# Performance work log

Measured on AMD Instinct MI355X. Metric: run time of the kernel, lower is better.

## Reference

```python
import jax, jax.numpy as jnp
import numpy as np

EMBED_DIM = 1024


def setup_inputs() -> dict:
    key = jax.random.key(0)
    ks = jax.random.split(key, 9)
    d = EMBED_DIM
    s = 1.0 / np.sqrt(d)
    return {
        "x": jax.random.normal(ks[0], (4, 2048, d), dtype=jnp.float32),
        "wq": jax.random.normal(ks[1], (d, d), dtype=jnp.float32) * s,
        "bq": jnp.zeros((d,), dtype=jnp.float32),
        "wk": jax.random.normal(ks[2], (d, d), dtype=jnp.float32) * s,
        "bk": jnp.zeros((d,), dtype=jnp.float32),
        "wv": jax.random.normal(ks[3], (d, d), dtype=jnp.float32) * s,
        "bv": jnp.zeros((d,), dtype=jnp.float32),
        "wo": jax.random.normal(ks[4], (d, d), dtype=jnp.float32) * s,
        "bo": jnp.zeros((d,), dtype=jnp.float32),
    }


def reference(x, wq, bq, wk, bk, wv, bv, wo, bo):
    # x: [B, S, D]; weights stored as [D_in, D_out] (torch Linear applies x @ W.T,
    # here we fold the transpose into storage).
    d = x.shape[-1]
    q = x @ wq + bq
    k = x @ wk + bk
    v = x @ wv + bv
    scores = jnp.einsum('bqd,bkd->bqk', q, k) / jnp.sqrt(jnp.float32(d))
    attn = jax.nn.softmax(scores, axis=-1)
    out = jnp.einsum('bqk,bkd->bqd', attn, v)
    return out @ wo + bo
```

## Files before the change

### kernel.cpp

```cpp
#include <hip/hip_runtime.h>
#include <stdint.h>

typedef __attribute__((ext_vector_type(4))) float f32x4;
typedef __attribute__((ext_vector_type(8))) short short8v;
typedef __attribute__((ext_vector_type(4))) unsigned short ushort4v;
typedef __attribute__((ext_vector_type(8))) unsigned short ushort8v;

__device__ __forceinline__ unsigned short f2b(float x) {
  union { float f; unsigned int u; } c; c.f = x;
  unsigned int r = (c.u + 0x7fffu + ((c.u >> 16) & 1u)) >> 16;
  return (unsigned short)r;
}

__device__ __forceinline__ void gload_lds16(const void* g, void* l) {
  __builtin_amdgcn_global_load_lds(
      (const __attribute__((address_space(1))) void*)g,
      (__attribute__((address_space(3))) void*)l, 16, 0, 0);
}

__device__ __forceinline__ f32x4 MFMA16(short8v a, short8v b, f32x4 c) {
  return __builtin_amdgcn_mfma_f32_16x16x32_bf16(a, b, c, 0, 0, 0);
}

template <int N>
__device__ __forceinline__ void wvm() {
  if constexpr (N == 8) asm volatile("s_waitcnt vmcnt(8)" ::: "memory");
  else if constexpr (N == 6) asm volatile("s_waitcnt vmcnt(6)" ::: "memory");
  else if constexpr (N == 4) asm volatile("s_waitcnt vmcnt(4)" ::: "memory");
  else if constexpr (N == 3) asm volatile("s_waitcnt vmcnt(3)" ::: "memory");
  else asm volatile("s_waitcnt vmcnt(0)" ::: "memory");
}

__global__ __launch_bounds__(256) void cvt_bf16(const float* __restrict__ in,
                                                unsigned short* __restrict__ out,
                                                int n8) {
  for (int i = blockIdx.x * 256 + threadIdx.x; i < n8; i += gridDim.x * 256) {
    f32x4 a = *((const f32x4*)in + (size_t)i * 2);
    f32x4 b = *((const f32x4*)in + (size_t)i * 2 + 1);
    ushort8v o;
    o[0] = f2b(a[0]); o[1] = f2b(a[1]); o[2] = f2b(a[2]); o[3] = f2b(a[3]);
    o[4] = f2b(b[0]); o[5] = f2b(b[1]); o[6] = f2b(b[2]); o[7] = f2b(b[3]);
    *((ushort8v*)out + i) = o;
  }
}

__global__ __launch_bounds__(256) void wt4_bf16(const float* __restrict__ w0,
                                                const float* __restrict__ w1,
                                                const float* __restrict__ w2,
                                                const float* __restrict__ w3,
                                                unsigned short* __restrict__ o0,
                                                unsigned short* __restrict__ o1,
                                                unsigned short* __restrict__ o2,
                                                unsigned short* __restrict__ o3) {
  const int z = blockIdx.z;
  const float* W = z == 0 ? w0 : z == 1 ? w1 : z == 2 ? w2 : w3;
  unsigned short* WT = z == 0 ? o0 : z == 1 ? o1 : z == 2 ? o2 : o3;
  __shared__ float t[64][65];
  const int bi = blockIdx.y * 64, bj = blockIdx.x * 64;
#pragma unroll
  for (int i = 0; i < 16; ++i) {
    int idx = i * 256 + threadIdx.x;
    int r = idx >> 6, c = idx & 63;
    t[r][c] = W[(size_t)(bi + r) * 1024 + bj + c];
  }
  __syncthreads();
#pragma unroll
  for (int i = 0; i < 16; ++i) {
    int idx = i * 256 + threadIdx.x;
    int r = idx >> 6, c = idx & 63;
    WT[(size_t)(bj + r) * 1024 + bi + c] = f2b(t[c][r]);
  }
}

__global__ __launch_bounds__(256) void softmax_rows(float* __restrict__ S,
                                                    long long bstride) {
  float* row = S + (long long)blockIdx.y * bstride + (size_t)blockIdx.x * 2048;
  const int t = threadIdx.x;
  f32x4 a = *(const f32x4*)(row + t * 8);
  f32x4 b = *(const f32x4*)(row + t * 8 + 4);
  float m = fmaxf(fmaxf(fmaxf(a[0], a[1]), fmaxf(a[2], a[3])),
                  fmaxf(fmaxf(b[0], b[1]), fmaxf(b[2], b[3])));
#pragma unroll
  for (int o = 32; o; o >>= 1) m = fmaxf(m, __shfl_xor(m, o));
  __shared__ float red[4];
  const int wid = t >> 6, lane = t & 63;
  if (lane == 0) red[wid] = m;
  __syncthreads();
  m = fmaxf(fmaxf(red[0], red[1]), fmaxf(red[2], red[3]));
  float e[8];
  float s = 0.f;
#pragma unroll
  for (int j = 0; j < 4; ++j) { e[j] = __expf(a[j] - m); s += e[j]; }
#pragma unroll
  for (int j = 0; j < 4; ++j) { e[4 + j] = __expf(b[j] - m); s += e[4 + j]; }
#pragma unroll
  for (int o = 32; o; o >>= 1) s += __shfl_xor(s, o);
  __syncthreads();
  if (lane == 0) red[wid] = s;
  __syncthreads();
  s = red[0] + red[1] + red[2] + red[3];
  const float inv = 1.f / s;
  ushort8v o8;
#pragma unroll
  for (int j = 0; j < 8; ++j) o8[j] = f2b(e[j] * inv);
  __syncthreads();
  *((ushort8v*)row + t) = o8;
}

__global__ __launch_bounds__(256, 2) void gemm_qkv128(
    const unsigned short* __restrict__ A,
    const unsigned short* __restrict__ B,
    unsigned short* __restrict__ Q, unsigned short* __restrict__ Kp,
    unsigned short* __restrict__ Vt,
    const float* __restrict__ bq, const float* __restrict__ bk,
    const float* __restrict__ bv) {
  __shared__ unsigned short As[128 * 32];
  __shared__ unsigned short Bs[128 * 32];
  const int tid = threadIdx.x;
  const int brow = blockIdx.y * 128, bcol = blockIdx.x * 128;
  const int wid = tid >> 6, lane = tid & 63;
  const int wr = (wid >> 1) * 64, wc = (wid & 1) * 64;
  const int lrow = lane & 15, kblk = lane >> 4;
  f32x4 acc[4][4] = {};
  for (int kk = 0; kk < 1024; kk += 32) {
#pragma unroll
    for (int r = 0; r < 2; ++r) {
      int idx = r * 256 + tid;
      int row = idx >> 2, seg = (idx & 3) * 8;
      gload_lds16(A + (size_t)(brow + row) * 1024 + kk + seg, (char*)As + idx * 16);
      gload_lds16(B + (size_t)(bcol + row) * 1024 + kk + seg, (char*)Bs + idx * 16);
    }
    __syncthreads();
    short8v af[4], bf[4];
#pragma unroll
    for (int m = 0; m < 4; ++m)
      af[m] = *(const short8v*)(As + (wr + m * 16 + lrow) * 32 + kblk * 8);
#pragma unroll
    for (int n = 0; n < 4; ++n)
      bf[n] = *(const short8v*)(Bs + (wc + n * 16 + lrow) * 32 + kblk * 8);
#pragma unroll
    for (int m = 0; m < 4; ++m)
#pragma unroll
      for (int n = 0; n < 4; ++n)
        acc[m][n] = MFMA16(af[m], bf[n], acc[m][n]);
    __syncthreads();
  }
  const int r0 = brow + wr + kblk * 4;
  const int c0 = bcol + wc + lrow;
  const int seg = bcol >> 10;
  if (seg < 2) {
    unsigned short* O = seg == 0 ? Q : Kp;
    const float* bb = seg == 0 ? bq : bk;
#pragma unroll
    for (int m = 0; m < 4; ++m)
#pragma unroll
      for (int n = 0; n < 4; ++n) {
        const int lc = c0 + n * 16 - seg * 1024;
        const float badd = bb[lc];
#pragma unroll
        for (int j = 0; j < 4; ++j)
          O[(size_t)(r0 + m * 16 + j) * 1024 + lc] = f2b(acc[m][n][j] + badd);
      }
  } else {
#pragma unroll
    for (int m = 0; m < 4; ++m)
#pragma unroll
      for (int n = 0; n < 4; ++n) {
        const int lc = c0 + n * 16 - 2048;
        const float badd = bv[lc];
        ushort4v pk;
#pragma unroll
        for (int j = 0; j < 4; ++j) pk[j] = f2b(acc[m][n][j] + badd);
        *(ushort4v*)(Vt + (size_t)lc * 8192 + r0 + m * 16) = pk;
      }
  }
}

template <int EPI, int BM>
__global__ __launch_bounds__(512, 2) void gemm256(
    const unsigned short* __restrict__ A, int lda,
    const unsigned short* __restrict__ B, int ldb,
    void* __restrict__ C0, void* __restrict__ C1, void* __restrict__ C2,
    int ldc, const float* __restrict__ bias0, const float* __restrict__ bias1,
    const float* __restrict__ bias2, float scale, int K,
    long long bsA, long long bsB, long long bsC) {
  extern __shared__ __align__(16) char smem[];
  constexpr int ABY = BM * 64;
  constexpr int KHS = ABY + 16384;
  constexpr int SBUF = 2 * KHS;
  constexpr int MF = BM / 32;
  constexpr int FH = MF / 2;
  constexpr int AL = BM / 128;
  constexpr int L = AL + 2;

  const int tid = threadIdx.x;
  const int z = blockIdx.z;
  A += (long long)z * bsA;
  B += (long long)z * bsB;
  const int blkrow = blockIdx.y * BM, blkcol = blockIdx.x * 256;
  const int lane = tid & 63, wid = tid >> 6;
  const int kblk = lane >> 4, l15 = lane & 15;
  const int arw = (wid >> 2) * (BM / 2) + l15;
  const int brw = (wid & 3) * 64 + l15;
  const int aoff = arw * 64 + ((kblk ^ ((arw >> 1) & 3)) << 4);
  const int boff = ABY + brw * 64 + ((kblk ^ ((brw >> 1) & 3)) << 4);
  const int srow = tid >> 2;
  const int scc = (((tid & 3) ^ ((srow >> 1) & 3)) << 3);
  const unsigned short* ag = A + (size_t)(blkrow + srow) * lda + scc;
  const unsigned short* bg = B + (size_t)(blkcol + srow) * ldb + scc;

  auto stA = [&](char* buf, int kt, int kh) {
    const unsigned short* g = ag + kt * 64 + kh * 32;
    char* l = buf + kh * KHS + tid * 16;
#pragma unroll
    for (int rr = 0; rr < AL; ++rr)
      gload_lds16(g + (size_t)(rr * 128) * lda, l + rr * 8192);
  };
  auto stB = [&](char* buf, int kt, int kh) {
    const unsigned short* g = bg + kt * 64 + kh * 32;
    char* l = buf + ABY + kh * KHS + tid * 16;
    gload_lds16(g, l);
    gload_lds16(g + (size_t)128 * ldb, l + 8192);
  };

  f32x4 acc[MF][4] = {};
  short8v af[4], bf[4];

#define LDAH(BUF, KK, MB)                                                     \
  { _Pragma("unroll") for (int m_ = 0; m_ < FH; ++m_)                         \
      af[m_] = *(const short8v*)((BUF) + (KK)*KHS + aoff + ((MB) + m_) * 1024); }
#define LDB4(BUF, KK)                                                         \
  { _Pragma("unroll") for (int n_ = 0; n_ < 4; ++n_)                          \
      bf[n_] = *(const short8v*)((BUF) + (KK)*KHS + boff + n_ * 1024); }
#define MMH(MH)                                                               \
  { _Pragma("unroll") for (int m_ = 0; m_ < FH; ++m_)                         \
      _Pragma("unroll") for (int n_ = 0; n_ < 4; ++n_)                        \
        acc[(MH)*FH + m_][n_] = MFMA16(af[m_], bf[n_], acc[(MH)*FH + m_][n_]); }
#define BAR __builtin_amdgcn_s_barrier()
#define WLGKM0 asm volatile("s_waitcnt lgkmcnt(0)" ::: "memory")

  const int NT = K >> 6;
  stA(smem, 0, 0); stB(smem, 0, 0); stA(smem, 0, 1); stB(smem, 0, 1);
  wvm<L>();
  BAR;
  for (int t = 0; t < NT; ++t) {
    char* cur = smem + (t & 1) * SBUF;
    char* nxt = smem + ((t + 1) & 1) * SBUF;
    const bool pf = (t + 1 < NT);
    LDAH(cur, 0, 0);
    LDB4(cur, 0);
    if (pf) { stA(nxt, t + 1, 0); stB(nxt, t + 1, 0); }
    BAR; WLGKM0;
    __builtin_amdgcn_s_setprio(1);
    MMH(0);
    __builtin_amdgcn_s_setprio(0);
    BAR;
    LDAH(cur, 0, FH);
    if (pf) { stA(nxt, t + 1, 1); stB(nxt, t + 1, 1); }
    BAR; WLGKM0;
    __builtin_amdgcn_s_setprio(1);
    MMH(1);
    __builtin_amdgcn_s_setprio(0);
    if (pf) wvm<2 * L>(); else wvm<0>();
    BAR;
    LDAH(cur, 1, 0);
    LDB4(cur, 1);
    BAR; WLGKM0;
    __builtin_amdgcn_s_setprio(1);
    MMH(0);
    __builtin_amdgcn_s_setprio(0);
    BAR;
    LDAH(cur, 1, FH);
    BAR; WLGKM0;
    __builtin_amdgcn_s_setprio(1);
    MMH(1);
    __builtin_amdgcn_s_setprio(0);
    if (pf) wvm<L>();
    BAR;
  }

  const int gr0 = blkrow + (wid >> 2) * (BM / 2) + kblk * 4;
  const int gc0 = blkcol + (wid & 3) * 64 + l15;
  if (EPI == 0) {
    float* C = (float*)C0 + (long long)z * bsC;
#pragma unroll
    for (int mi = 0; mi < MF; ++mi)
#pragma unroll
      for (int n = 0; n < 4; ++n) {
        const int gc = gc0 + n * 16;
        const float badd = bias0 ? bias0[gc] : 0.f;
#pragma unroll
        for (int j = 0; j < 4; ++j)
          C[(size_t)(gr0 + mi * 16 + j) * ldc + gc] = acc[mi][n][j] * scale + badd;
      }
  } else if (EPI == 1) {
    unsigned short* C = (unsigned short*)C0 + (long long)z * bsC;
#pragma unroll
    for (int mi = 0; mi < MF; ++mi)
#pragma unroll
      for (int n = 0; n < 4; ++n) {
        const int gc = gc0 + n * 16;
        const float badd = bias0 ? bias0[gc] : 0.f;
#pragma unroll
        for (int j = 0; j < 4; ++j)
          C[(size_t)(gr0 + mi * 16 + j) * ldc + gc] = f2b(acc[mi][n][j] * scale + badd);
      }
  } else {
    const int seg = blkcol >> 10;
#pragma unroll
    for (int mi = 0; mi < MF; ++mi)
#pragma unroll
      for (int n = 0; n < 4; ++n) {
        const int gc = gc0 + n * 16;
        const int lc = gc - seg * 1024;
        if (seg < 2) {
          unsigned short* O = (unsigned short*)(seg == 0 ? C0 : C1);
          const float* bb = (seg == 0 ? bias0 : bias1);
          const float badd = bb[lc];
#pragma unroll
          for (int j = 0; j < 4; ++j)
            O[(size_t)(gr0 + mi * 16 + j) * 1024 + lc] = f2b(acc[mi][n][j] + badd);
        } else {
          unsigned short* O = (unsigned short*)C2;
          const float badd = bias2[lc];
          ushort4v pk;
#pragma unroll
          for (int j = 0; j < 4; ++j) pk[j] = f2b(acc[mi][n][j] + badd);
          *(ushort4v*)(O + (size_t)lc * 8192 + gr0 + mi * 16) = pk;
        }
      }
  }
#undef LDAH
#undef LDB4
#undef MMH
#undef BAR
#undef WLGKM0
}

template <int OMODE, bool BIAS, bool SCALE>
__global__ __launch_bounds__(256, 2) void gemm_bt(
    const unsigned short* __restrict__ A, int lda,
    const unsigned short* __restrict__ B, int ldb,
    void* __restrict__ Cp, int ldc,
    const float* __restrict__ bias, float scale, int K,
    long long bsA, long long bsB, long long bsC) {
  __shared__ unsigned short As[128 * 32];
  __shared__ unsigned short Bs[128 * 32];
  const int tid = threadIdx.x;
  A += (long long)blockIdx.z * bsA;
  B += (long long)blockIdx.z * bsB;
  const int brow = blockIdx.y * 128, bcol = blockIdx.x * 128;
  const int wid = tid >> 6, lane = tid & 63;
  const int wr = (wid >> 1) * 64, wc = (wid & 1) * 64;
  const int lrow = lane & 15, kblk = lane >> 4;
  f32x4 acc[4][4] = {};
  for (int kk = 0; kk < K; kk += 32) {
#pragma unroll
    for (int r = 0; r < 2; ++r) {
      int idx = r * 256 + tid;
      int row = idx >> 2, seg = (idx & 3) * 8;
      gload_lds16(A + (size_t)(brow + row) * lda + kk + seg, (char*)As + idx * 16);
      gload_lds16(B + (size_t)(bcol + row) * ldb + kk + seg, (char*)Bs + idx * 16);
    }
    __syncthreads();
    short8v af[4], bv[4];
#pragma unroll
    for (int m = 0; m < 4; ++m)
      af[m] = *(const short8v*)(As + (wr + m * 16 + lrow) * 32 + kblk * 8);
#pragma unroll
    for (int n = 0; n < 4; ++n)
      bv[n] = *(const short8v*)(Bs + (wc + n * 16 + lrow) * 32 + kblk * 8);
#pragma unroll
    for (int m = 0; m < 4; ++m)
#pragma unroll
      for (int n = 0; n < 4; ++n)
        acc[m][n] = MFMA16(af[m], bv[n], acc[m][n]);
    __syncthreads();
  }
  const int r0 = brow + wr + kblk * 4;
  const int c0 = bcol + wc + lrow;
  if (OMODE == 0) {
    float* C = (float*)Cp + (long long)blockIdx.z * bsC;
#pragma unroll
    for (int m = 0; m < 4; ++m)
#pragma unroll
      for (int n = 0; n < 4; ++n) {
        const int cc = c0 + n * 16;
        const float badd = BIAS ? bias[cc] : 0.f;
#pragma unroll
        for (int j = 0; j < 4; ++j) {
          float v = acc[m][n][j];
          if (SCALE) v *= scale;
          C[(size_t)(r0 + m * 16 + j) * ldc + cc] = v + badd;
        }
      }
  } else if (OMODE == 1) {
    unsigned short* C = (unsigned short*)Cp + (long long)blockIdx.z * bsC;
#pragma unroll
    for (int m = 0; m < 4; ++m)
#pragma unroll
      for (int n = 0; n < 4; ++n) {
        const int cc = c0 + n * 16;
        const float badd = BIAS ? bias[cc] : 0.f;
#pragma unroll
        for (int j = 0; j < 4; ++j) {
          float v = acc[m][n][j];
          if (SCALE) v *= scale;
          C[(size_t)(r0 + m * 16 + j) * ldc + cc] = f2b(v + badd);
        }
      }
  } else {
    unsigned short* C = (unsigned short*)Cp + (long long)blockIdx.z * bsC;
#pragma unroll
    for (int m = 0; m < 4; ++m)
#pragma unroll
      for (int n = 0; n < 4; ++n) {
        const int cc = c0 + n * 16;
        const float badd = BIAS ? bias[cc] : 0.f;
        ushort4v pk;
#pragma unroll
        for (int j = 0; j < 4; ++j) {
          float v = acc[m][n][j];
          if (SCALE) v *= scale;
          pk[j] = f2b(v + badd);
        }
        *(ushort4v*)(C + (size_t)cc * ldc + (r0 + m * 16)) = pk;
      }
  }
}

extern "C" void kernel_launch(void* const* d_in, const int* in_sizes, int n_in,
                              void* d_out, int out_size, void* d_ws, size_t ws_size,
                              hipStream_t stream) {
  const float* x  = (const float*)d_in[0];
  const float* wq = (const float*)d_in[1];
  const float* bq = (const float*)d_in[2];
  const float* wk = (const float*)d_in[3];
  const float* bk = (const float*)d_in[4];
  const float* wv = (const float*)d_in[5];
  const float* bv = (const float*)d_in[6];
  const float* wo = (const float*)d_in[7];
  const float* bo = (const float*)d_in[8];
  float* out = (float*)d_out;
  char* ws = (char*)d_ws;

  const long long WELEM = 1024LL * 1024;
  const long long BATCH = 2048LL * 1024;
  const long long FULL  = 4 * BATCH;
  const long long SELEM = 2048LL * 2048;

  const size_t need_A = 8388608ull + 5ull * 16777216 + 4ull * 16777216;
  const size_t need_C = 8388608ull + 4ull * 4194304 + 16777216ull;

  if (ws_size >= need_A) {
    unsigned short* wqT = (unsigned short*)ws;
    unsigned short* wkT = wqT + WELEM;
    unsigned short* wvT = wkT + WELEM;
    unsigned short* woT = wvT + WELEM;
    unsigned short* xb  = woT + WELEM;
    unsigned short* qb  = xb + FULL;
    unsigned short* kb  = qb + FULL;
    unsigned short* vt  = kb + FULL;
    unsigned short* ao  = vt + FULL;
    float* S = (float*)(ao + FULL);

    hipFuncSetAttribute(reinterpret_cast<const void*>(&gemm256<0, 256>),
                        hipFuncAttributeMaxDynamicSharedMemorySize, 131072);
    hipFuncSetAttribute(reinterpret_cast<const void*>(&gemm256<1, 128>),
                        hipFuncAttributeMaxDynamicSharedMemorySize, 98304);
    hipFuncSetAttribute(reinterpret_cast<const void*>(&gemm256<0, 128>),
                        hipFuncAttributeMaxDynamicSharedMemorySize, 98304);

    cvt_bf16<<<2048, 256, 0, stream>>>(x, xb, (int)(FULL / 8));
    wt4_bf16<<<dim3(16, 16, 4), 256, 0, stream>>>(wq, wk, wv, wo, wqT, wkT, wvT, woT);

    gemm_qkv128<<<dim3(24, 64), 256, 0, stream>>>(
        xb, wqT, qb, kb, vt, bq, bk, bv);
    gemm256<0, 256><<<dim3(8, 8, 4), 512, 131072, stream>>>(
        qb, 1024, kb, 1024, S, nullptr, nullptr, 2048, nullptr, nullptr,
        nullptr, 0.03125f, 1024, BATCH, BATCH, SELEM);
    softmax_rows<<<dim3(2048, 4), 256, 0, stream>>>(S, SELEM);
    gemm256<1, 128><<<dim3(4, 16, 4), 512, 98304, stream>>>(
        (const unsigned short*)S, 4096, vt, 8192, ao, nullptr, nullptr, 1024,
        nullptr, nullptr, nullptr, 1.f, 2048, 2 * SELEM, 2048, BATCH);
    gemm256<0, 128><<<dim3(4, 64, 1), 512, 98304, stream>>>(
        ao, 1024, woT, 1024, out, nullptr, nullptr, 1024, bo, nullptr, nullptr,
        1.f, 1024, 0, 0, 0);
  } else if (ws_size >= need_C) {
    unsigned short* wqT = (unsigned short*)ws;
    unsigned short* wkT = wqT + WELEM;
    unsigned short* wvT = wkT + WELEM;
    unsigned short* woT = wvT + WELEM;
    unsigned short* xb  = woT + WELEM;
    unsigned short* qb  = xb + BATCH;
    unsigned short* kb  = qb + BATCH;
    unsigned short* vtb = kb + BATCH;
    float* S = (float*)(vtb + BATCH);

    wt4_bf16<<<dim3(16, 16, 4), 256, 0, stream>>>(wq, wk, wv, wo, wqT, wkT, wvT, woT);

    for (int b = 0; b < 4; ++b) {
      cvt_bf16<<<1024, 256, 0, stream>>>(x + b * BATCH, xb, (int)(BATCH / 8));
      dim3 gqkv(8, 16);
      gemm_bt<1, true, false><<<gqkv, 256, 0, stream>>>(xb, 1024, wqT, 1024, qb, 1024, bq, 1.f, 1024, 0, 0, 0);
      gemm_bt<1, true, false><<<gqkv, 256, 0, stream>>>(xb, 1024, wkT, 1024, kb, 1024, bk, 1.f, 1024, 0, 0, 0);
      gemm_bt<2, true, false><<<gqkv, 256, 0, stream>>>(xb, 1024, wvT, 1024, vtb, 2048, bv, 1.f, 1024, 0, 0, 0);
      gemm_bt<0, false, true><<<dim3(16, 16), 256, 0, stream>>>(
          qb, 1024, kb, 1024, S, 2048, nullptr, 0.03125f, 1024, 0, 0, 0);
      softmax_rows<<<dim3(2048, 1), 256, 0, stream>>>(S, 0);
      gemm_bt<1, false, false><<<dim3(8, 16), 256, 0, stream>>>(
          (const unsigned short*)S, 4096, vtb, 2048, xb, 1024, nullptr, 1.f, 2048, 0, 0, 0);
      gemm_bt<0, true, false><<<dim3(8, 16), 256, 0, stream>>>(
          xb, 1024, woT, 1024, out + b * BATCH, 1024, bo, 1.f, 1024, 0, 0, 0);
    }
  }
}
```

Baseline: 212.9 us.

## Store attention scores in bf16 and widen QKV GEMM K-tile with swizzled LDS

The score GEMM now writes bf16 scores instead of fp32, and a new softmax kernel reads and writes bf16 in place. This halves score-matrix traffic for the softmax and for the PV GEMM's input stride. Separately, the QKV GEMM loads 64-wide K tiles with an XOR swizzle in LDS, halving barrier iterations and avoiding bank conflicts. Rounding scores to bf16 before softmax adds precision loss in the logits.

```diff
diff --git a/kernel.cpp b/kernel.cpp
--- a/kernel.cpp
+++ b/kernel.cpp
@@ -10,6 +10,11 @@
   union { float f; unsigned int u; } c; c.f = x;
   unsigned int r = (c.u + 0x7fffu + ((c.u >> 16) & 1u)) >> 16;
   return (unsigned short)r;
+}
+
+__device__ __forceinline__ float b2f(unsigned short x) {
+  union { unsigned int u; float f; } c; c.u = ((unsigned int)x) << 16;
+  return c.f;
 }
 
 __device__ __forceinline__ void gload_lds16(const void* g, void* l) {
@@ -72,6 +77,40 @@
   }
 }
 
+__global__ __launch_bounds__(256) void softmax_bf16(unsigned short* __restrict__ S,
+                                                    long long bstride) {
+  unsigned short* row = S + (long long)blockIdx.y * bstride + (size_t)blockIdx.x * 2048;
+  const int t = threadIdx.x;
+  ushort8v u = *((const ushort8v*)row + t);
+  float v[8];
+#pragma unroll
+  for (int j = 0; j < 8; ++j) v[j] = b2f(u[j]);
+  float m = v[0];
+#pragma unroll
+  for (int j = 1; j < 8; ++j) m = fmaxf(m, v[j]);
+#pragma unroll
+  for (int o = 32; o; o >>= 1) m = fmaxf(m, __shfl_xor(m, o));
+  __shared__ float red[4];
+  const int wid = t >> 6, lane = t & 63;
+  if (lane == 0) red[wid] = m;
+  __syncthreads();
+  m = fmaxf(fmaxf(red[0], red[1]), fmaxf(red[2], red[3]));
+  float s = 0.f;
+#pragma unroll
+  for (int j = 0; j < 8; ++j) { v[j] = __expf(v[j] - m); s += v[j]; }
+#pragma unroll
+  for (int o = 32; o; o >>= 1) s += __shfl_xor(s, o);
+  __syncthreads();
+  if (lane == 0) red[wid] = s;
+  __syncthreads();
+  s = red[0] + red[1] + red[2] + red[3];
+  const float inv = 1.f / s;
+  ushort8v o8;
+#pragma unroll
+  for (int j = 0; j < 8; ++j) o8[j] = f2b(v[j] * inv);
+  *((ushort8v*)row + t) = o8;
+}
+
 __global__ __launch_bounds__(256) void softmax_rows(float* __restrict__ S,
                                                     long long bstride) {
   float* row = S + (long long)blockIdx.y * bstride + (size_t)blockIdx.x * 2048;
@@ -114,35 +153,44 @@
     unsigned short* __restrict__ Vt,
     const float* __restrict__ bq, const float* __restrict__ bk,
     const float* __restrict__ bv) {
-  __shared__ unsigned short As[128 * 32];
-  __shared__ unsigned short Bs[128 * 32];
+  __shared__ unsigned short As[128 * 64];
+  __shared__ unsigned short Bs[128 * 64];
   const int tid = threadIdx.x;
   const int brow = blockIdx.y * 128, bcol = blockIdx.x * 128;
   const int wid = tid >> 6, lane = tid & 63;
   const int wr = (wid >> 1) * 64, wc = (wid & 1) * 64;
   const int lrow = lane & 15, kblk = lane >> 4;
   f32x4 acc[4][4] = {};
-  for (int kk = 0; kk < 1024; kk += 32) {
-#pragma unroll
-    for (int r = 0; r < 2; ++r) {
-      int idx = r * 256 + tid;
-      int row = idx >> 2, seg = (idx & 3) * 8;
-      gload_lds16(A + (size_t)(brow + row) * 1024 + kk + seg, (char*)As + idx * 16);
-      gload_lds16(B + (size_t)(bcol + row) * 1024 + kk + seg, (char*)Bs + idx * 16);
+  for (int kk = 0; kk < 1024; kk += 64) {
+#pragma unroll
+    for (int g = 0; g < 4; ++g) {
+      int idx = g * 256 + tid;
+      int row = idx >> 3;
+      int lk8 = ((idx & 7) ^ (row & 7)) << 3;
+      gload_lds16(A + (size_t)(brow + row) * 1024 + kk + lk8, (char*)As + idx * 16);
+      gload_lds16(B + (size_t)(bcol + row) * 1024 + kk + lk8, (char*)Bs + idx * 16);
     }
     __syncthreads();
-    short8v af[4], bf[4];
-#pragma unroll
-    for (int m = 0; m < 4; ++m)
-      af[m] = *(const short8v*)(As + (wr + m * 16 + lrow) * 32 + kblk * 8);
-#pragma unroll
-    for (int n = 0; n < 4; ++n)
-      bf[n] = *(const short8v*)(Bs + (wc + n * 16 + lrow) * 32 + kblk * 8);
-#pragma unroll
-    for (int m = 0; m < 4; ++m)
-#pragma unroll
-      for (int n = 0; n < 4; ++n)
-        acc[m][n] = MFMA16(af[m], bf[n], acc[m][n]);
+#pragma unroll
+    for (int ks = 0; ks < 2; ++ks) {
+      short8v af[4], bf[4];
+      const int kc = ks * 4 + kblk;
+#pragma unroll
+      for (int m = 0; m < 4; ++m) {
+        const int row = wr + m * 16 + lrow;
+        af[m] = *(const short8v*)(As + row * 64 + ((kc ^ (row & 7)) << 3));
+      }
+#pragma unroll
+      for (int n = 0; n < 4; ++n) {
+        const int row = wc + n * 16 + lrow;
+        bf[n] = *(const short8v*)(Bs + row * 64 + ((kc ^ (row & 7)) << 3));
+      }
+#pragma unroll
+      for (int m = 0; m < 4; ++m)
+#pragma unroll
+        for (int n = 0; n < 4; ++n)
+          acc[m][n] = MFMA16(af[m], bf[n], acc[m][n]);
+    }
     __syncthreads();
   }
   const int r0 = brow + wr + kblk * 4;
@@ -462,9 +510,9 @@
     unsigned short* kb  = qb + FULL;
     unsigned short* vt  = kb + FULL;
     unsigned short* ao  = vt + FULL;
-    float* S = (float*)(ao + FULL);
-
-    hipFuncSetAttribute(reinterpret_cast<const void*>(&gemm256<0, 256>),
+    unsigned short* S   = ao + FULL;
+
+    hipFuncSetAttribute(reinterpret_cast<const void*>(&gemm256<1, 256>),
                         hipFuncAttributeMaxDynamicSharedMemorySize, 131072);
     hipFuncSetAttribute(reinterpret_cast<const void*>(&gemm256<1, 128>),
                         hipFuncAttributeMaxDynamicSharedMemorySize, 98304);
@@ -476,13 +524,13 @@
 
     gemm_qkv128<<<dim3(24, 64), 256, 0, stream>>>(
         xb, wqT, qb, kb, vt, bq, bk, bv);
-    gemm256<0, 256><<<dim3(8, 8, 4), 512, 131072, stream>>>(
+    gemm256<1, 256><<<dim3(8, 8, 4), 512, 131072, stream>>>(
         qb, 1024, kb, 1024, S, nullptr, nullptr, 2048, nullptr, nullptr,
         nullptr, 0.03125f, 1024, BATCH, BATCH, SELEM);
-    softmax_rows<<<dim3(2048, 4), 256, 0, stream>>>(S, SELEM);
+    softmax_bf16<<<dim3(2048, 4), 256, 0, stream>>>(S, SELEM);
     gemm256<1, 128><<<dim3(4, 16, 4), 512, 98304, stream>>>(
-        (const unsigned short*)S, 4096, vt, 8192, ao, nullptr, nullptr, 1024,
-        nullptr, nullptr, nullptr, 1.f, 2048, 2 * SELEM, 2048, BATCH);
+        S, 2048, vt, 8192, ao, nullptr, nullptr, 1024,
+        nullptr, nullptr, nullptr, 1.f, 2048, SELEM, 2048, BATCH);
     gemm256<0, 128><<<dim3(4, 64, 1), 512, 98304, stream>>>(
         ao, 1024, woT, 1024, out, nullptr, nullptr, 1024, bo, nullptr, nullptr,
         1.f, 1024, 0, 0, 0);
```

Measured after the change: 194.5 us. 8.6% less time.
